# Performance work log

Measured on AMD Instinct MI355X. Metric: run time of the kernel, lower is better.

The kernel has to match this reference:

```python
import jax, jax.numpy as jnp
import numpy as np

# module hyperparameters (from init_kwargs)
R_MIN, R_MAX = 0.01, 0.6
RH, RW = 64, 64          # retinal_H, retinal_W
H, W = 64, 128           # output pooled H, W
UFR, UFT = 4, 4          # upsampling factors


def make_grid(weight):
    """Vectorized version of get_grid. weight: [B,2].
    Faithful to source: only the top-left [H, W] corner of the
    [H*UFR, W*UFT] grid is written; the rest (torch.empty in the
    original) is set to 0 here for determinism."""
    i = jnp.arange(H, dtype=jnp.float32)
    j = jnp.arange(W, dtype=jnp.float32)
    xg = (i - (H // 2)) / (H / 2.0)
    yg = (j - (W // 2)) / (W / 2.0)
    xx, yy = jnp.meshgrid(xg, yg, indexing="ij")  # [H,W]
    # clamp radius to avoid log(0) = -inf at the center pixel; the resulting
    # coordinate is far out of [-1,1] and gets border-clamped either way.
    logr = jnp.log(jnp.maximum(jnp.sqrt(xx ** 2 + yy ** 2), 1e-12))  # [H,W]
    lo = jnp.log(weight[:, 0] * R_MIN)[:, None, None]  # [B,1,1]
    hi = jnp.log(weight[:, 1] * R_MAX)[:, None, None]  # [B,1,1]
    r = RH * (logr[None] - lo) / (hi - lo)             # [B,H,W]
    a = jnp.arctan2(yy, xx)
    a = jnp.where(a > 0, a, 2.0 * np.pi + a)
    t = 0.5 * a * RW / np.pi                           # [H,W]
    gx = jnp.broadcast_to((t / (RW / 2.0) - 1.0)[None], r.shape)
    gy = r / (RH / 2.0) - 1.0
    small = jnp.stack([gx, gy], axis=-1)               # [B,H,W,2]
    grid = jnp.zeros((weight.shape[0], H * UFR, W * UFT, 2), jnp.float32)
    return grid.at[:, :H, :W, :].set(small)


def grid_sample_border(x, grid):
    """torch.F.grid_sample, mode=bilinear, padding_mode=border, align_corners=False.
    x: [B,C,Hin,Win], grid: [B,Hg,Wg,2] -> [B,C,Hg,Wg]."""
    B, C, Hin, Win = x.shape
    gx, gy = grid[..., 0], grid[..., 1]
    ix = jnp.clip(((gx + 1.0) * Win - 1.0) * 0.5, 0.0, Win - 1.0)
    iy = jnp.clip(((gy + 1.0) * Hin - 1.0) * 0.5, 0.0, Hin - 1.0)
    x0f = jnp.floor(ix)
    y0f = jnp.floor(iy)
    wx = (ix - x0f)[..., None]
    wy = (iy - y0f)[..., None]
    x0 = jnp.clip(x0f.astype(jnp.int32), 0, Win - 1)
    y0 = jnp.clip(y0f.astype(jnp.int32), 0, Hin - 1)
    x1 = jnp.clip(x0 + 1, 0, Win - 1)
    y1 = jnp.clip(y0 + 1, 0, Hin - 1)
    bidx = jnp.arange(B)[:, None, None]
    gather = lambda yi, xi: x[bidx, :, yi, xi]  # [B,Hg,Wg,C]
    out = (gather(y0, x0) * (1 - wx) * (1 - wy)
           + gather(y0, x1) * wx * (1 - wy)
           + gather(y1, x0) * (1 - wx) * wy
           + gather(y1, x1) * wx * wy)
    return jnp.transpose(out, (0, 3, 1, 2))  # [B,C,Hg,Wg]


def setup_inputs() -> dict:
    key = jax.random.key(0)
    k1, k2, k3, k4, k5, k6 = jax.random.split(key, 6)
    B, C, Hin, Win = 8, 64, 224, 224
    Cmid = C // 2  # int(channel * r)
    return {
        "x": jax.random.normal(k1, (B, C, Hin, Win), jnp.float32),
        "l_t_prev": jax.random.uniform(k2, (B, 2), jnp.float32),
        "w1": jax.random.normal(k3, (C, Cmid), jnp.float32) * 0.1,
        "b1": jnp.zeros((Cmid,), jnp.float32),
        "w2": jax.random.normal(k4, (Cmid, 2), jnp.float32) * 0.1,
        "b2": jnp.zeros((2,), jnp.float32),
    }


def reference(x, l_t_prev, w1, b1, w2, b2):
    # att: global avg pool -> fc -> sigmoid
    branch = x.mean(axis=(2, 3))                              # [B,C]
    weight = jax.nn.sigmoid(jax.nn.relu(branch @ w1 + b1) @ w2 + b2)  # [B,2]
    grid = make_grid(weight) + l_t_prev[:, None, None, :]     # [B,Hg,Wg,2]
    sampled = grid_sample_border(x, grid)                     # [B,C,Hg,Wg]
    B, C = sampled.shape[:2]
    pooled = sampled.reshape(B, C, H, UFR, W, UFT).mean(axis=(3, 5))  # AvgPool2d([UFR,UFT])
    return pooled, weight
```

## Files before the change

kernel.cpp:

```cpp
#include <hip/hip_runtime.h>
#include <math.h>

#define B 8
#define C 64
#define HIN 224
#define WIN 224
#define PLANE (HIN*WIN)
#define PLANE4 (PLANE/4)
#define QUART (PLANE4/4)
#define OH 64
#define OW 128
#define OUT_PER_BC (OH*OW)
#define NGRID (OH*OW)
#define POOLED_SIZE (B*C*OH*OW)

#define WS_PARTIAL 0
#define WS_COORDS 4096

#define PI_F 3.14159265358979323846f

__device__ __forceinline__ float bilinear(const float* __restrict__ p,
                                          float ix, float iy) {
    float x0f = floorf(ix), y0f = floorf(iy);
    int x0 = (int)x0f, y0 = (int)y0f;
    float wx = ix - x0f, wy = iy - y0f;
    int x1 = min(x0 + 1, WIN - 1);
    int y1 = min(y0 + 1, HIN - 1);
    const float* r0 = p + y0 * WIN;
    const float* r1 = p + y1 * WIN;
    float v00 = r0[x0], v01 = r0[x1], v10 = r1[x0], v11 = r1[x1];
    float v0 = v00 + (v01 - v00) * wx;
    float v1 = v10 + (v11 - v10) * wx;
    return v0 + (v1 - v0) * wy;
}

__global__ __launch_bounds__(256) void k1_gap_fill(const float* __restrict__ x,
                                                   const float* __restrict__ l_t,
                                                   float* __restrict__ ws,
                                                   float* __restrict__ out) {
    int blk = blockIdx.x;
    int bc  = blk >> 2, q = blk & 3;
    const float* plane = x + (size_t)bc * PLANE;
    const float4* p = (const float4*)plane + q * QUART;
    int tid = threadIdx.x;
    float s = 0.f;
#pragma unroll
    for (int k = 0; k < 12; ++k) {
        float4 v = p[tid + k * 256];
        s += (v.x + v.y) + (v.z + v.w);
    }
    if (tid < QUART - 12 * 256) {
        float4 v = p[tid + 12 * 256];
        s += (v.x + v.y) + (v.z + v.w);
    }

    {
        int b = bc >> 6;
        float gx = l_t[2 * b], gy = l_t[2 * b + 1];
        float ixc = fminf(fmaxf(((gx + 1.f) * (float)WIN - 1.f) * 0.5f, 0.f), (float)(WIN - 1));
        float iyc = fminf(fmaxf(((gy + 1.f) * (float)HIN - 1.f) * 0.5f, 0.f), (float)(HIN - 1));
        float vc = bilinear(plane, ixc, iyc);
        float4 v4 = make_float4(vc, vc, vc, vc);
        float4* o4 = (float4*)(out + (size_t)bc * OUT_PER_BC);
        int end = q * 480 + 480;
        for (int it = q * 480 + tid; it < end; it += 256) {
            int off;
            if (it < 384) {
                int r = it / 24;
                off = r * 32 + 8 + (it - r * 24);
            } else {
                int t2 = it - 384;
                off = (16 + (t2 >> 5)) * 32 + (t2 & 31);
            }
            o4[off] = v4;
        }
    }

    for (int off = 32; off; off >>= 1) s += __shfl_down(s, off, 64);
    __shared__ float lds[4];
    if ((tid & 63) == 0) lds[tid >> 6] = s;
    __syncthreads();
    if (tid == 0) ws[WS_PARTIAL + blk] = lds[0] + lds[1] + lds[2] + lds[3];
}

__global__ __launch_bounds__(256) void k2_coords(const float* __restrict__ w1,
                                                 const float* __restrict__ b1,
                                                 const float* __restrict__ w2,
                                                 const float* __restrict__ b2,
                                                 const float* __restrict__ l_t,
                                                 float* __restrict__ ws,
                                                 float* __restrict__ out_weight) {
    __shared__ float branch[B * C];
    __shared__ float hidden[256];
    __shared__ float wv[16];
    int tid = threadIdx.x;
    for (int i = tid; i < B * C; i += 256) {
        const float* pp = ws + WS_PARTIAL + i * 4;
        branch[i] = (pp[0] + pp[1] + pp[2] + pp[3]) * (1.0f / PLANE);
    }
    __syncthreads();
    {
        int bb = tid >> 5, m = tid & 31;
        float h = b1[m];
#pragma unroll 8
        for (int c = 0; c < C; ++c) h += branch[bb * C + c] * w1[c * 32 + m];
        hidden[tid] = fmaxf(h, 0.f);
    }
    __syncthreads();
    if (tid < 16) {
        int bb = tid >> 1, k = tid & 1;
        float s = b2[k];
#pragma unroll
        for (int m = 0; m < 32; ++m) s += hidden[bb * 32 + m] * w2[m * 2 + k];
        float v = 1.f / (1.f + expf(-s));
        wv[tid] = v;
        if (blockIdx.x == 0) out_weight[tid] = v;
    }
    __syncthreads();

    int p = blockIdx.x * 256 + tid;
    int b = p >> 13;
    int rem = p & 8191;
    int i = rem >> 7;
    int j = rem & 127;
    float lo = logf(wv[b * 2 + 0] * 0.01f);
    float hi = logf(wv[b * 2 + 1] * 0.6f);
    float xg = (float)(i - 32) * (1.f / 32.f);
    float yg = (float)(j - 64) * (1.f / 64.f);
    float rr = sqrtf(xg * xg + yg * yg);
    float logr = logf(fmaxf(rr, 1e-12f));
    float r = 64.f * (logr - lo) / (hi - lo);
    float a = atan2f(yg, xg);
    if (!(a > 0.f)) a = 2.f * PI_F + a;
    float t = 0.5f * a * 64.f / PI_F;
    float gx = t * (1.f / 32.f) - 1.f + l_t[b * 2 + 0];
    float gy = r * (1.f / 32.f) - 1.f + l_t[b * 2 + 1];
    float ix = ((gx + 1.f) * (float)WIN - 1.f) * 0.5f;
    float iy = ((gy + 1.f) * (float)HIN - 1.f) * 0.5f;
    ix = fminf(fmaxf(ix, 0.f), (float)(WIN - 1));
    iy = fminf(fmaxf(iy, 0.f), (float)(HIN - 1));
    ((float2*)(ws + WS_COORDS))[p] = make_float2(ix, iy);
}

__global__ __launch_bounds__(256) void k3_corner(const float* __restrict__ x,
                                                 const float2* __restrict__ coords,
                                                 float* __restrict__ out) {
    int o = blockIdx.x * 256 + threadIdx.x;
    int b = o >> 15;
    int c = (o >> 9) & 63;
    int h = (o >> 5) & 15;
    int w = o & 31;
    const float* plane = x + (size_t)((b << 6) | c) * PLANE;
    const float2* cb = coords + ((size_t)b << 13);
    float acc = 0.f;
#pragma unroll
    for (int di = 0; di < 4; ++di) {
        const float4* cr = (const float4*)(cb + ((4 * h + di) << 7) + (w << 2));
        float4 q0 = cr[0];
        float4 q1 = cr[1];
        acc += bilinear(plane, q0.x, q0.y);
        acc += bilinear(plane, q0.z, q0.w);
        acc += bilinear(plane, q1.x, q1.y);
        acc += bilinear(plane, q1.z, q1.w);
    }
    out[((size_t)((b << 6) | c) << 13) + (h << 7) + w] = acc * (1.f / 16.f);
}

extern "C" void kernel_launch(void* const* d_in, const int* in_sizes, int n_in,
                              void* d_out, int out_size, void* d_ws, size_t ws_size,
                              hipStream_t stream) {
    const float* x   = (const float*)d_in[0];
    const float* l_t = (const float*)d_in[1];
    const float* w1  = (const float*)d_in[2];
    const float* b1  = (const float*)d_in[3];
    const float* w2  = (const float*)d_in[4];
    const float* b2  = (const float*)d_in[5];
    float* out = (float*)d_out;
    float* ws  = (float*)d_ws;

    k1_gap_fill<<<dim3(B * C * 4), dim3(256), 0, stream>>>(x, l_t, ws, out);
    k2_coords<<<dim3(256), dim3(256), 0, stream>>>(w1, b1, w2, b2, l_t, ws,
                                                   out + POOLED_SIZE);
    k3_corner<<<dim3(1024), dim3(256), 0, stream>>>(x, (const float2*)(ws + WS_COORDS), out);
}
```

Baseline: 180.3 us.

## Fuse coordinate computation into corner sampling kernel via shared memory

```diff
diff --git a/kernel.cpp b/kernel.cpp
--- a/kernel.cpp
+++ b/kernel.cpp
@@ -11,11 +11,9 @@
 #define OH 64
 #define OW 128
 #define OUT_PER_BC (OH*OW)
-#define NGRID (OH*OW)
 #define POOLED_SIZE (B*C*OH*OW)
 
 #define WS_PARTIAL 0
-#define WS_COORDS 4096
 
 #define PI_F 3.14159265358979323846f
 
@@ -83,17 +81,24 @@
     if (tid == 0) ws[WS_PARTIAL + blk] = lds[0] + lds[1] + lds[2] + lds[3];
 }
 
-__global__ __launch_bounds__(256) void k2_coords(const float* __restrict__ w1,
-                                                 const float* __restrict__ b1,
-                                                 const float* __restrict__ w2,
-                                                 const float* __restrict__ b2,
-                                                 const float* __restrict__ l_t,
-                                                 float* __restrict__ ws,
-                                                 float* __restrict__ out_weight) {
+__global__ __launch_bounds__(256) void k2_fused(const float* __restrict__ x,
+                                                const float* __restrict__ w1,
+                                                const float* __restrict__ b1,
+                                                const float* __restrict__ w2,
+                                                const float* __restrict__ b2,
+                                                const float* __restrict__ l_t,
+                                                const float* __restrict__ ws,
+                                                float* __restrict__ out,
+                                                float* __restrict__ out_weight) {
+    __shared__ float2 scoords[4096];
     __shared__ float branch[B * C];
     __shared__ float hidden[256];
     __shared__ float wv[16];
     int tid = threadIdx.x;
+    int bc = blockIdx.x >> 1;
+    int b  = bc >> 6;
+    int h0 = (blockIdx.x & 1) * 8;
+
     for (int i = tid; i < B * C; i += 256) {
         const float* pp = ws + WS_PARTIAL + i * 4;
         branch[i] = (pp[0] + pp[1] + pp[2] + pp[3]) * (1.0f / PLANE);
@@ -118,52 +123,48 @@
     }
     __syncthreads();
 
-    int p = blockIdx.x * 256 + tid;
-    int b = p >> 13;
-    int rem = p & 8191;
-    int i = rem >> 7;
-    int j = rem & 127;
     float lo = logf(wv[b * 2 + 0] * 0.01f);
     float hi = logf(wv[b * 2 + 1] * 0.6f);
-    float xg = (float)(i - 32) * (1.f / 32.f);
-    float yg = (float)(j - 64) * (1.f / 64.f);
-    float rr = sqrtf(xg * xg + yg * yg);
-    float logr = logf(fmaxf(rr, 1e-12f));
-    float r = 64.f * (logr - lo) / (hi - lo);
-    float a = atan2f(yg, xg);
-    if (!(a > 0.f)) a = 2.f * PI_F + a;
-    float t = 0.5f * a * 64.f / PI_F;
-    float gx = t * (1.f / 32.f) - 1.f + l_t[b * 2 + 0];
-    float gy = r * (1.f / 32.f) - 1.f + l_t[b * 2 + 1];
-    float ix = ((gx + 1.f) * (float)WIN - 1.f) * 0.5f;
-    float iy = ((gy + 1.f) * (float)HIN - 1.f) * 0.5f;
-    ix = fminf(fmaxf(ix, 0.f), (float)(WIN - 1));
-    iy = fminf(fmaxf(iy, 0.f), (float)(HIN - 1));
-    ((float2*)(ws + WS_COORDS))[p] = make_float2(ix, iy);
-}
+    float ltx = l_t[b * 2 + 0], lty = l_t[b * 2 + 1];
+#pragma unroll
+    for (int k = 0; k < 16; ++k) {
+        int s = tid + k * 256;
+        int gr = s >> 7;
+        int dj = (s >> 5) & 3;
+        int w  = s & 31;
+        int i = h0 * 4 + gr;
+        int j = w * 4 + dj;
+        float xg = (float)(i - 32) * (1.f / 32.f);
+        float yg = (float)(j - 64) * (1.f / 64.f);
+        float rr = sqrtf(xg * xg + yg * yg);
+        float logr = logf(fmaxf(rr, 1e-12f));
+        float r = 64.f * (logr - lo) / (hi - lo);
+        float a = atan2f(yg, xg);
+        if (!(a > 0.f)) a = 2.f * PI_F + a;
+        float t = 0.5f * a * 64.f / PI_F;
+        float gx = t * (1.f / 32.f) - 1.f + ltx;
+        float gy = r * (1.f / 32.f) - 1.f + lty;
+        float ix = ((gx + 1.f) * (float)WIN - 1.f) * 0.5f;
+        float iy = ((gy + 1.f) * (float)HIN - 1.f) * 0.5f;
+        ix = fminf(fmaxf(ix, 0.f), (float)(WIN - 1));
+        iy = fminf(fmaxf(iy, 0.f), (float)(HIN - 1));
+        scoords[s] = make_float2(ix, iy);
+    }
+    __syncthreads();
 
-__global__ __launch_bounds__(256) void k3_corner(const float* __restrict__ x,
-                                                 const float2* __restrict__ coords,
-                                                 float* __restrict__ out) {
-    int o = blockIdx.x * 256 + threadIdx.x;
-    int b = o >> 15;
-    int c = (o >> 9) & 63;
-    int h = (o >> 5) & 15;
-    int w = o & 31;
-    const float* plane = x + (size_t)((b << 6) | c) * PLANE;
-    const float2* cb = coords + ((size_t)b << 13);
+    const float* plane = x + (size_t)bc * PLANE;
+    int hr = tid >> 5;
+    int w  = tid & 31;
     float acc = 0.f;
 #pragma unroll
     for (int di = 0; di < 4; ++di) {
-        const float4* cr = (const float4*)(cb + ((4 * h + di) << 7) + (w << 2));
-        float4 q0 = cr[0];
-        float4 q1 = cr[1];
-        acc += bilinear(plane, q0.x, q0.y);
-        acc += bilinear(plane, q0.z, q0.w);
-        acc += bilinear(plane, q1.x, q1.y);
-        acc += bilinear(plane, q1.z, q1.w);
+#pragma unroll
+        for (int dj = 0; dj < 4; ++dj) {
+            float2 cxy = scoords[(hr * 4 + di) * 128 + dj * 32 + w];
+            acc += bilinear(plane, cxy.x, cxy.y);
+        }
     }
-    out[((size_t)((b << 6) | c) << 13) + (h << 7) + w] = acc * (1.f / 16.f);
+    out[((size_t)bc << 13) + ((h0 + hr) << 7) + w] = acc * (1.f / 16.f);
 }
 
 extern "C" void kernel_launch(void* const* d_in, const int* in_sizes, int n_in,
@@ -179,7 +180,6 @@
     float* ws  = (float*)d_ws;
 
     k1_gap_fill<<<dim3(B * C * 4), dim3(256), 0, stream>>>(x, l_t, ws, out);
-    k2_coords<<<dim3(256), dim3(256), 0, stream>>>(w1, b1, w2, b2, l_t, ws,
-                                                   out + POOLED_SIZE);
-    k3_corner<<<dim3(1024), dim3(256), 0, stream>>>(x, (const float2*)(ws + WS_COORDS), out);
+    k2_fused<<<dim3(1024), dim3(256), 0, stream>>>(x, w1, b1, w2, b2, l_t, ws,
+                                                   out, out + POOLED_SIZE);
 }
```

After: 184.6 us. 2.4% more time.
